# Optimization experiments

Measured on AMD Instinct MI355X. Metric: run time of the kernel, lower is better.

The kernel has to match this reference:

```python
import jax, jax.numpy as jnp
import numpy as np

TEMP = 0.07
MAX_SAMPLES = 2048
RADIUS = 10
HARD_FRAC = 0.75
FG_LABEL = 1
B, C, H, W = 8, 64, 256, 256
BLOCK = 32

MAX_FG = MAX_SAMPLES // 2                      # 1024
NEG_BUDGET = MAX_SAMPLES - MAX_FG              # 1024
HARD_BUDGET = int(round(HARD_FRAC * NEG_BUDGET))  # 768
RAND_BUDGET = NEG_BUDGET - HARD_BUDGET         # 256


def setup_inputs() -> dict:
    key = jax.random.key(0)
    feats = jax.random.normal(key, (B, C, H, W), dtype=jnp.float32)
    # 32x32-block checkerboard labels: guarantees abundant fg / ring / interior-bg pools
    ii, jj = jnp.meshgrid(jnp.arange(H), jnp.arange(W), indexing='ij')
    lbl = (((ii // BLOCK) + (jj // BLOCK)) % 2).astype(jnp.int32)
    labels = jnp.broadcast_to(lbl, (B, H, W))
    return {"feats": feats, "labels": labels}


def _forward(feats, labels):
    Bn, Cn, Hn, Wn = feats.shape
    n_pix = Hn * Wn
    f_flat = feats.reshape(Bn, Cn, n_pix).transpose(0, 2, 1)  # [B, P, C]
    l_flat = labels.reshape(Bn, n_pix)

    fg = labels == FG_LABEL                                   # [B, H, W]
    k = 2 * RADIUS + 1
    # max-pool dilation of fg mask (kernel k, stride 1, pad RADIUS == SAME)
    dil = jax.lax.reduce_window(fg.astype(jnp.float32), -jnp.inf, jax.lax.max,
                                (1, k, k), (1, 1, 1), 'SAME') > 0.0
    fg_flat = fg.reshape(Bn, n_pix)
    bg_flat = ~fg_flat                                        # all pixels valid (no ignore)
    ring_flat = dil.reshape(Bn, n_pix) & ~fg_flat & bg_flat
    bgonly_flat = bg_flat & ~ring_flat

    def per_image(f, y, fgm, ringm, bgm, key):
        k1, k2, k3 = jax.random.split(key, 3)
        def pick(mask, kk, n):
            # random subset of n true positions (== randperm[:n] in distribution)
            s = jnp.where(mask, jax.random.uniform(kk, mask.shape), -1.0)
            return jax.lax.top_k(s, n)[1]
        idx = jnp.concatenate([pick(fgm, k1, MAX_FG),
                               pick(ringm, k2, HARD_BUDGET),
                               pick(bgm, k3, RAND_BUDGET)])    # [K]
        fs = f[idx]                                            # [K, C]
        ys = y[idx]
        fs = fs / jnp.maximum(jnp.linalg.norm(fs, axis=1, keepdims=True), 1e-12)
        logits = fs @ fs.T / TEMP                              # [K, K]
        logits = logits - jax.lax.stop_gradient(logits.max(axis=1, keepdims=True))
        eye = jnp.eye(MAX_SAMPLES, dtype=bool)
        pos = (ys[:, None] == ys[None, :]) & ~eye
        exp_l = jnp.exp(logits) * (~eye)
        denom = jnp.maximum(exp_l.sum(axis=1), 1e-8)
        pos_sum = jnp.maximum(jnp.where(pos, exp_l, 0.0).sum(axis=1), 1e-8)
        valid = pos.any(axis=1) & (ys == FG_LABEL)
        loss_terms = -jnp.log(pos_sum / denom)
        n_valid = jnp.maximum(valid.sum(), 1)
        return jnp.where(valid, loss_terms, 0.0).sum() / n_valid

    keys = jax.random.split(jax.random.key(1), Bn)
    losses = jax.vmap(per_image)(f_flat, l_flat, fg_flat, ring_flat, bgonly_flat, keys)
    return losses.mean()


def reference(feats, labels):
    return _forward(feats, labels)
```

## Files before the change

### kernel.cpp

```cpp
#include <hip/hip_runtime.h>
#include <stdint.h>

#define NPIX   65536
#define NIMG   8
#define NCH    64
#define KSEL   2048
#define NFG    1024
#define NRING  768
#define NBG    256
#define INV_TEMP 14.285714285714286f

typedef __attribute__((ext_vector_type(8))) short bf16x8;
typedef __attribute__((ext_vector_type(4))) float f32x4;

__device__ __forceinline__ void tf2x32(uint32_t k0, uint32_t k1,
                                       uint32_t& x0, uint32_t& x1) {
  const uint32_t ks2 = k0 ^ k1 ^ 0x1BD11BDAu;
  x0 += k0; x1 += k1;
#define TF_RND(r) { x0 += x1; x1 = (x1 << (r)) | (x1 >> (32 - (r))); x1 ^= x0; }
  TF_RND(13) TF_RND(15) TF_RND(26) TF_RND(6)
  x0 += k1;  x1 += ks2 + 1u;
  TF_RND(17) TF_RND(29) TF_RND(16) TF_RND(24)
  x0 += ks2; x1 += k0 + 2u;
  TF_RND(13) TF_RND(15) TF_RND(26) TF_RND(6)
  x0 += k0;  x1 += k1 + 3u;
  TF_RND(17) TF_RND(29) TF_RND(16) TF_RND(24)
  x0 += k1;  x1 += ks2 + 4u;
  TF_RND(13) TF_RND(15) TF_RND(26) TF_RND(6)
  x0 += ks2; x1 += k0 + 5u;
#undef TF_RND
}

__device__ __forceinline__ ushort f2bf(float f) {
  uint32_t u = __float_as_uint(f);
  return (ushort)((u + 0x7FFFu + ((u >> 16) & 1u)) >> 16);
}

__global__ __launch_bounds__(256) void prep_hash(const int* __restrict__ labels,
                                                 float4* __restrict__ zreg,
                                                 uint32_t* __restrict__ mgrp,
                                                 uint32_t* __restrict__ hist32,
                                                 float* __restrict__ out) {
  __shared__ uint64_t fgs[112], hds[112], fgb[32], dlb[32];
  __shared__ uint32_t lh[768];
  __shared__ uint32_t skeys[6];
  const int tid = threadIdx.x;
  const int img = blockIdx.x >> 5;
  const int band = blockIdx.x & 31;

  if (blockIdx.x == 0) {
    if (tid < 16) zreg[tid] = make_float4(0.f, 0.f, 0.f, 0.f);
    if (tid == 0) out[0] = 0.0f;
  }

  if (tid < 3) {
    uint32_t kb0 = 0u, kb1 = (uint32_t)img;
    tf2x32(0u, 1u, kb0, kb1);
    uint32_t x0 = 0u, x1 = (uint32_t)tid;
    tf2x32(kb0, kb1, x0, x1);
    skeys[tid * 2 + 0] = x0;
    skeys[tid * 2 + 1] = x1;
  }
  for (int t = tid; t < 768; t += 256) lh[t] = 0;

  const int rbase = band * 8 - 10;
  for (int it = 0; it < 28; ++it) {
    int hr = rbase + it;
    bool bit = false;
    if (hr >= 0 && hr < 256) bit = (labels[(img << 16) + (hr << 8) + tid] == 1);
    uint64_t m = __ballot(bit);
    if ((tid & 63) == 0) fgs[it * 4 + (tid >> 6)] = m;
  }
  __syncthreads();

  for (int w = tid; w < 112; w += 256) {
    int wc = w & 3;
    uint64_t x = fgs[w];
    uint64_t L = wc > 0 ? fgs[w - 1] : 0ull;
    uint64_t R = wc < 3 ? fgs[w + 1] : 0ull;
    uint64_t acc = x;
    #pragma unroll
    for (int s = 1; s <= 10; ++s) {
      acc |= (x << s) | (L >> (64 - s));
      acc |= (x >> s) | (R << (64 - s));
    }
    hds[w] = acc;
  }
  __syncthreads();

  for (int w = tid; w < 32; w += 256) {
    int r = w >> 2, wc = w & 3;
    uint64_t acc = 0ull;
    #pragma unroll
    for (int dr = 0; dr <= 20; ++dr) acc |= hds[(r + dr) * 4 + wc];
    fgb[w] = fgs[(r + 10) * 4 + wc];
    dlb[w] = acc;
  }
  __syncthreads();

  const uint32_t K00 = skeys[0], K01 = skeys[1];
  const uint32_t K10 = skeys[2], K11 = skeys[3];
  const uint32_t K20 = skeys[4], K21 = skeys[5];
  const int pbase = blockIdx.x * 2048;

  #pragma unroll
  for (int k = 0; k < 8; ++k) {
    int off = k * 256 + tid;
    int pix = (pbase + off) & 65535;
    int lw = off >> 6, bp = off & 63;
    uint32_t fgbit = (uint32_t)((fgb[lw] >> bp) & 1ull);
    uint32_t dilbit = (uint32_t)((dlb[lw] >> bp) & 1ull);
    uint32_t grp = fgbit ? 0u : (dilbit ? 1u : 2u);
    uint32_t k0 = grp == 0 ? K00 : grp == 1 ? K10 : K20;
    uint32_t k1 = grp == 0 ? K01 : grp == 1 ? K11 : K21;
    uint32_t x0 = 0u, x1 = (uint32_t)pix;
    tf2x32(k0, k1, x0, x1);
    uint32_t m = (x0 ^ x1) >> 9;
    mgrp[pbase + off] = (m << 2) | grp;
    atomicAdd(&lh[grp * 256 + (m >> 15)], 1u);
  }
  __syncthreads();
  for (int t = tid; t < 768; t += 256) hist32[blockIdx.x * 768 + t] = lh[t];
}

__global__ __launch_bounds__(256) void topk_emit(const uint32_t* __restrict__ mgrp,
                                                 const uint32_t* __restrict__ hist32,
                                                 uint32_t* __restrict__ TG,
                                                 uint32_t* __restrict__ cnt,
                                                 uint32_t* __restrict__ candcnt,
                                                 unsigned long long* __restrict__ cand,
                                                 int* __restrict__ idx_out) {
  __shared__ uint32_t hh[768];
  __shared__ uint32_t sT[3], loc[3], lbd[3], basA[3], basB[3];
  const int tid = threadIdx.x;
  const int b = blockIdx.x >> 5;
  const int base = blockIdx.x * 2048;
  for (int t = tid; t < 768; t += 256) {
    uint32_t s = 0;
    const uint32_t* hp = hist32 + (size_t)b * 32 * 768 + t;
    #pragma unroll
    for (int band = 0; band < 32; ++band) s += hp[band * 768];
    hh[t] = s;
  }
  if (tid < 3) { loc[tid] = 0; lbd[tid] = 0; }
  __syncthreads();

  if (tid < 3) {
    uint32_t nsel = tid == 0 ? NFG : tid == 1 ? NRING : NBG;
    const uint32_t* h = hh + tid * 256;
    uint32_t cum = 0; int T = 255;
    for (; T > 0; --T) {
      uint32_t c = h[T];
      if (cum + c >= nsel) break;
      cum += c;
    }
    sT[tid] = (uint32_t)T;
    if ((blockIdx.x & 31) == 0) {
      TG[(b * 3 + tid) * 2] = (uint32_t)T;
      TG[(b * 3 + tid) * 2 + 1] = cum;
    }
  }
  __syncthreads();
  const uint32_t T0 = sT[0], T1 = sT[1], T2 = sT[2];

  #pragma unroll
  for (int k = 0; k < 8; ++k) {
    uint32_t v = mgrp[base + k * 256 + tid];
    uint32_t g = v & 3u, bin = v >> 17;
    uint32_t T = g == 0 ? T0 : g == 1 ? T1 : T2;
    if (bin > T) atomicAdd(&loc[g], 1u);
    else if (bin == T) atomicAdd(&lbd[g], 1u);
  }
  __syncthreads();
  if (tid < 3) {
    basA[tid] = atomicAdd(&cnt[b * 3 + tid], loc[tid]);
    basB[tid] = atomicAdd(&candcnt[b * 3 + tid], lbd[tid]);
    loc[tid] = 0; lbd[tid] = 0;
  }
  __syncthreads();

  #pragma unroll
  for (int k = 0; k < 8; ++k) {
    int p = base + k * 256 + tid;
    uint32_t v = mgrp[p];
    uint32_t g = v & 3u, bin = v >> 17;
    uint32_t T = g == 0 ? T0 : g == 1 ? T1 : T2;
    int pix = p & 65535;
    if (bin > T) {
      uint32_t o = atomicAdd(&loc[g], 1u);
      int seg = g == 0 ? 0 : g == 1 ? NFG : (NFG + NRING);
      idx_out[b * KSEL + seg + (int)(basA[g] + o)] = pix;
    } else if (bin == T) {
      uint32_t o = atomicAdd(&lbd[g], 1u);
      uint32_t c = basB[g] + o;
      uint32_t m = v >> 2;
      if (c < 1024u)
        cand[((size_t)b * 3 + g) * 1024 + c] =
            ((unsigned long long)m << 16) | (uint32_t)pix;
    }
  }
}

#define GA 16
__global__ __launch_bounds__(256) void gather_rank_t(
    const float* __restrict__ feats, const int* __restrict__ idx,
    const uint32_t* __restrict__ TG, const uint32_t* __restrict__ candcnt,
    const unsigned long long* __restrict__ cand, ushort* __restrict__ fs) {
  __shared__ float tile[GA * 65];
  __shared__ float ssb[16 * GA];
  __shared__ float sscale[GA];
  __shared__ int lidx[GA];
  __shared__ unsigned long long cb[1024];
  const int tid = threadIdx.x;
  const int img = blockIdx.x >> 7;
  const int win = (blockIdx.x & 127) * GA;
  int seg, segoff, nsel;
  if (win < NFG)               { seg = 0; segoff = 0;            nsel = NFG; }
  else if (win < NFG + NRING)  { seg = 1; segoff = NFG;          nsel = NRING; }
  else                         { seg = 2; segoff = NFG + NRING;  nsel = NBG; }
  const int task = img * 3 + seg;
  const uint32_t G = TG[task * 2 + 1];
  const int poslo = win - segoff;

  if (tid < GA) {
    if ((uint32_t)(poslo + tid) < G)
      lidx[tid] = idx[img * KSEL + win + tid];
  }
  const bool needRank = (uint32_t)(poslo + GA) > G;
  if (needRank) {
    const int c = (int)(candcnt[task] < 1024u ? candcnt[task] : 1024u);
    const int r = nsel - (int)G;
    for (int i = tid; i < c; i += 256) cb[i] = cand[task * 1024 + i];
    __syncthreads();
    for (int i = tid; i < c; i += 256) {
      unsigned long long me = cb[i];
      uint32_t mm = (uint32_t)(me >> 16), pi = (uint32_t)(me & 0xFFFFu);
      int rank = 0;
      for (int j = 0; j < c; ++j) {
        unsigned long long o = cb[j];
        uint32_t om = (uint32_t)(o >> 16), op = (uint32_t)(o & 0xFFFFu);
        if (om > mm || (om == mm && op < pi)) ++rank;
      }
      if (rank < r) {
        int slot = (int)G + rank - poslo;
        if (slot >= 0 && slot < GA) lidx[slot] = (int)pi;
      }
    }
  }
  __syncthreads();

  const int a = tid & 15, q = tid >> 4;
  const int pix = lidx[a];
  const float* fb = feats + ((size_t)img * NCH + q * 4) * NPIX + pix;
  float ss = 0.f;
  #pragma unroll
  for (int k = 0; k < 4; ++k) {
    float v = fb[(size_t)k * NPIX];
    tile[a * 65 + q * 4 + k] = v;
    ss += v * v;
  }
  ssb[q * GA + a] = ss;
  __syncthreads();
  if (q == 0) {
    float tot = 0.f;
    #pragma unroll
    for (int q2 = 0; q2 < 16; ++q2) tot += ssb[q2 * GA + a];
    sscale[a] = 1.0f / fmaxf(sqrtf(tot), 1e-12f);
  }
  __syncthreads();

  const int row = tid >> 4, c4 = tid & 15;
  const float sc = sscale[row];
  ushort4 v4;
  v4.x = f2bf(tile[row * 65 + c4 * 4 + 0] * sc);
  v4.y = f2bf(tile[row * 65 + c4 * 4 + 1] * sc);
  v4.z = f2bf(tile[row * 65 + c4 * 4 + 2] * sc);
  v4.w = f2bf(tile[row * 65 + c4 * 4 + 3] * sc);
  ((ushort4*)(fs + ((size_t)img * KSEL + win + row) * NCH))[c4] = v4;
}

__global__ __launch_bounds__(256) void loss_mfma(const ushort* __restrict__ fs,
                                                 float* __restrict__ out) {
  const int img = blockIdx.x & 7;
  const int a0 = (blockIdx.x >> 3) * 32;
  const ushort* X = fs + (size_t)img * KSEL * NCH;
  const int tid = threadIdx.x;
  const int lane = tid & 63, wave = tid >> 6;
  const int quad = lane >> 4, col = lane & 15;
  const int rt = wave >> 1, colh = wave & 1;

  __shared__ float redD[2][2][16];
  __shared__ float redP[2][16];

  const int arow = a0 + rt * 16 + col;
  const bf16x8* Ap = (const bf16x8*)(X + (size_t)arow * NCH + quad * 8);
  const bf16x8 a_lo = Ap[0];
  const bf16x8 a_hi = Ap[4];

  float pD[4] = {0.f, 0.f, 0.f, 0.f};
  float pP[4] = {0.f, 0.f, 0.f, 0.f};
  const int ct0 = colh * 64;
  const int mbase = a0 + rt * 16 + quad * 4;

  for (int ct = ct0; ct < ct0 + 64; ++ct) {
    const int j = ct * 16 + col;
    const bf16x8* Bp = (const bf16x8*)(X + (size_t)j * NCH + quad * 8);
    bf16x8 b_lo = Bp[0];
    bf16x8 b_hi = Bp[4];
    f32x4 d = {0.f, 0.f, 0.f, 0.f};
    d = __builtin_amdgcn_mfma_f32_16x16x32_bf16(a_lo, b_lo, d, 0, 0, 0);
    d = __builtin_amdgcn_mfma_f32_16x16x32_bf16(a_hi, b_hi, d, 0, 0, 0);
    #pragma unroll
    for (int r = 0; r < 4; ++r) {
      float e = __expf(d[r] * INV_TEMP);
      if (j == mbase + r) e = 0.f;
      pD[r] += e;
      if (colh == 0) pP[r] += e;
    }
  }

  #pragma unroll
  for (int o = 1; o < 16; o <<= 1) {
    #pragma unroll
    for (int r = 0; r < 4; ++r) {
      pD[r] += __shfl_xor(pD[r], o);
      pP[r] += __shfl_xor(pP[r], o);
    }
  }
  if (col == 0) {
    #pragma unroll
    for (int r = 0; r < 4; ++r) {
      redD[rt][colh][quad * 4 + r] = pD[r];
      if (colh == 0) redP[rt][quad * 4 + r] = pP[r];
    }
  }
  __syncthreads();

  float term = 0.f;
  if (tid < 32) {
    int lrt = tid >> 4, lr = tid & 15;
    float dsum = fmaxf(redD[lrt][0][lr] + redD[lrt][1][lr], 1e-8f);
    float psum = fmaxf(redP[lrt][lr], 1e-8f);
    term = __logf(dsum) - __logf(psum);
  }
  if (tid < 64) {
    #pragma unroll
    for (int o = 32; o > 0; o >>= 1) term += __shfl_xor(term, o);
    if (tid == 0) atomicAdd(out, term * (1.0f / (NFG * NIMG)));
  }
}

extern "C" void kernel_launch(void* const* d_in, const int* in_sizes, int n_in,
                              void* d_out, int out_size, void* d_ws, size_t ws_size,
                              hipStream_t stream) {
  const float* feats = (const float*)d_in[0];
  const int* labels  = (const int*)d_in[1];
  float* out = (float*)d_out;

  char* ws = (char*)d_ws;
  uint32_t* TG      = (uint32_t*)(ws);
  uint32_t* cnt     = (uint32_t*)(ws + 4096);
  uint32_t* candcnt = (uint32_t*)(ws + 4224);
  float4*   zreg    = (float4*)(ws + 4096);
  unsigned long long* cand = (unsigned long long*)(ws + 8192);
  int*      idx     = (int*)(ws + 262144);
  uint32_t* mgrp    = (uint32_t*)(ws + 2097152);
  uint32_t* hist32  = (uint32_t*)(ws + 4194304);
  ushort*   fs      = (ushort*)(ws + 8388608);

  hipLaunchKernelGGL(prep_hash, dim3(NIMG * 32), dim3(256), 0, stream,
                     labels, zreg, mgrp, hist32, out);
  hipLaunchKernelGGL(topk_emit, dim3(NIMG * 32), dim3(256), 0, stream,
                     mgrp, hist32, TG, cnt, candcnt, cand, idx);
  hipLaunchKernelGGL(gather_rank_t, dim3((NIMG * KSEL) / GA), dim3(256), 0, stream,
                     feats, idx, TG, candcnt, cand, fs);
  hipLaunchKernelGGL(loss_mfma, dim3(NIMG * (NFG / 32)), dim3(256), 0, stream,
                     fs, out);
}
```

Measured before the change: 239.9 us.

## Replace global atomic compaction with histogram prefix offsets and widen loss blocks

topk_emit now derives each band's output offsets from per-band histograms (a prefix over bands) and uses wave ballots plus popcount for ordered in-block compaction. This replaces the global atomic counters and the second pass over mgrp, and writes candcnt directly, so the zeroing of counters in prep_hash is dropped. loss_mfma moves to 1024-thread blocks with 8 column segments per row tile, giving each wave a quarter of the column loop to raise parallelism. The compaction adds two block barriers per iteration, and output order becomes deterministic.

```diff
diff --git a/kernel.cpp b/kernel.cpp
--- a/kernel.cpp
+++ b/kernel.cpp
@@ -37,7 +37,6 @@
 }
 
 __global__ __launch_bounds__(256) void prep_hash(const int* __restrict__ labels,
-                                                 float4* __restrict__ zreg,
                                                  uint32_t* __restrict__ mgrp,
                                                  uint32_t* __restrict__ hist32,
                                                  float* __restrict__ out) {
@@ -48,10 +47,7 @@
   const int img = blockIdx.x >> 5;
   const int band = blockIdx.x & 31;
 
-  if (blockIdx.x == 0) {
-    if (tid < 16) zreg[tid] = make_float4(0.f, 0.f, 0.f, 0.f);
-    if (tid == 0) out[0] = 0.0f;
-  }
+  if (blockIdx.x == 0 && tid == 0) out[0] = 0.0f;
 
   if (tid < 3) {
     uint32_t kb0 = 0u, kb1 = (uint32_t)img;
@@ -126,23 +122,31 @@
 __global__ __launch_bounds__(256) void topk_emit(const uint32_t* __restrict__ mgrp,
                                                  const uint32_t* __restrict__ hist32,
                                                  uint32_t* __restrict__ TG,
-                                                 uint32_t* __restrict__ cnt,
                                                  uint32_t* __restrict__ candcnt,
                                                  unsigned long long* __restrict__ cand,
                                                  int* __restrict__ idx_out) {
   __shared__ uint32_t hh[768];
-  __shared__ uint32_t sT[3], loc[3], lbd[3], basA[3], basB[3];
+  __shared__ uint32_t sT[3];
+  __shared__ uint32_t cA[3][32], cB[3][32];
+  __shared__ uint32_t preA[3], preB[3];
+  __shared__ uint32_t runA[3], runB[3];
+  __shared__ uint32_t wcA[3][4], wcB[3][4];
   const int tid = threadIdx.x;
   const int b = blockIdx.x >> 5;
+  const int band = blockIdx.x & 31;
   const int base = blockIdx.x * 2048;
+
+  uint32_t vv[8];
+  #pragma unroll
+  for (int k = 0; k < 8; ++k) vv[k] = mgrp[base + k * 256 + tid];
+
   for (int t = tid; t < 768; t += 256) {
     uint32_t s = 0;
-    const uint32_t* hp = hist32 + (size_t)b * 32 * 768 + t;
-    #pragma unroll
-    for (int band = 0; band < 32; ++band) s += hp[band * 768];
+    const uint32_t* hp = hist32 + (size_t)b * 24576 + t;
+    #pragma unroll
+    for (int bd = 0; bd < 32; ++bd) s += hp[bd * 768];
     hh[t] = s;
   }
-  if (tid < 3) { loc[tid] = 0; lbd[tid] = 0; }
   __syncthreads();
 
   if (tid < 3) {
@@ -155,49 +159,83 @@
       cum += c;
     }
     sT[tid] = (uint32_t)T;
-    if ((blockIdx.x & 31) == 0) {
+    runA[tid] = 0; runB[tid] = 0;
+    if (band == 0) {
       TG[(b * 3 + tid) * 2] = (uint32_t)T;
       TG[(b * 3 + tid) * 2 + 1] = cum;
+      candcnt[b * 3 + tid] = h[T];
     }
   }
   __syncthreads();
   const uint32_t T0 = sT[0], T1 = sT[1], T2 = sT[2];
 
-  #pragma unroll
+  if (tid < 96) {
+    int g = tid >> 5, bd = tid & 31;
+    uint32_t T = g == 0 ? T0 : g == 1 ? T1 : T2;
+    const uint32_t* hp = hist32 + (size_t)b * 24576 + bd * 768 + g * 256;
+    uint32_t sA = 0;
+    for (int t = (int)T + 1; t < 256; ++t) sA += hp[t];
+    cA[g][bd] = sA;
+    cB[g][bd] = hp[T];
+  }
+  __syncthreads();
+  if (tid < 3) {
+    uint32_t pa = 0, pb = 0;
+    for (int bd = 0; bd < band; ++bd) { pa += cA[tid][bd]; pb += cB[tid][bd]; }
+    preA[tid] = pa; preB[tid] = pb;
+  }
+  __syncthreads();
+
+  const int lane = tid & 63, w = tid >> 6;
+  #pragma unroll 1
   for (int k = 0; k < 8; ++k) {
-    uint32_t v = mgrp[base + k * 256 + tid];
-    uint32_t g = v & 3u, bin = v >> 17;
-    uint32_t T = g == 0 ? T0 : g == 1 ? T1 : T2;
-    if (bin > T) atomicAdd(&loc[g], 1u);
-    else if (bin == T) atomicAdd(&lbd[g], 1u);
-  }
-  __syncthreads();
-  if (tid < 3) {
-    basA[tid] = atomicAdd(&cnt[b * 3 + tid], loc[tid]);
-    basB[tid] = atomicAdd(&candcnt[b * 3 + tid], lbd[tid]);
-    loc[tid] = 0; lbd[tid] = 0;
-  }
-  __syncthreads();
-
-  #pragma unroll
-  for (int k = 0; k < 8; ++k) {
-    int p = base + k * 256 + tid;
-    uint32_t v = mgrp[p];
-    uint32_t g = v & 3u, bin = v >> 17;
-    uint32_t T = g == 0 ? T0 : g == 1 ? T1 : T2;
-    int pix = p & 65535;
-    if (bin > T) {
-      uint32_t o = atomicAdd(&loc[g], 1u);
-      int seg = g == 0 ? 0 : g == 1 ? NFG : (NFG + NRING);
-      idx_out[b * KSEL + seg + (int)(basA[g] + o)] = pix;
-    } else if (bin == T) {
-      uint32_t o = atomicAdd(&lbd[g], 1u);
-      uint32_t c = basB[g] + o;
-      uint32_t m = v >> 2;
-      if (c < 1024u)
-        cand[((size_t)b * 3 + g) * 1024 + c] =
-            ((unsigned long long)m << 16) | (uint32_t)pix;
-    }
+    const uint32_t v = vv[k];
+    const uint32_t g = v & 3u, bin = v >> 17;
+    const uint32_t T = g == 0 ? T0 : g == 1 ? T1 : T2;
+    const bool selA = bin > T;
+    const bool selB = bin == T;
+    const uint64_t mA0 = __ballot(selA && g == 0);
+    const uint64_t mA1 = __ballot(selA && g == 1);
+    const uint64_t mA2 = __ballot(selA && g == 2);
+    const uint64_t mB0 = __ballot(selB && g == 0);
+    const uint64_t mB1 = __ballot(selB && g == 1);
+    const uint64_t mB2 = __ballot(selB && g == 2);
+    if (lane == 0) {
+      wcA[0][w] = (uint32_t)__popcll(mA0);
+      wcA[1][w] = (uint32_t)__popcll(mA1);
+      wcA[2][w] = (uint32_t)__popcll(mA2);
+      wcB[0][w] = (uint32_t)__popcll(mB0);
+      wcB[1][w] = (uint32_t)__popcll(mB1);
+      wcB[2][w] = (uint32_t)__popcll(mB2);
+    }
+    __syncthreads();
+    if (selA || selB) {
+      const uint64_t mask = g == 0 ? (selA ? mA0 : mB0)
+                          : g == 1 ? (selA ? mA1 : mB1)
+                                   : (selA ? mA2 : mB2);
+      const uint32_t intra = (uint32_t)__popcll(mask & ((1ull << lane) - 1ull));
+      uint32_t wbase = 0;
+      for (int w2 = 0; w2 < w; ++w2) wbase += selA ? wcA[g][w2] : wcB[g][w2];
+      const int pix = (base + k * 256 + tid) & 65535;
+      if (selA) {
+        const uint32_t slot = preA[g] + runA[g] + wbase + intra;
+        const int seg = g == 0 ? 0 : g == 1 ? NFG : (NFG + NRING);
+        idx_out[b * KSEL + seg + (int)slot] = pix;
+      } else {
+        const uint32_t c = preB[g] + runB[g] + wbase + intra;
+        if (c < 1024u) {
+          const uint32_t m = v >> 2;
+          cand[((size_t)b * 3 + g) * 1024 + c] =
+              ((unsigned long long)m << 16) | (uint32_t)pix;
+        }
+      }
+    }
+    __syncthreads();
+    if (tid < 3) {
+      runA[tid] += wcA[tid][0] + wcA[tid][1] + wcA[tid][2] + wcA[tid][3];
+      runB[tid] += wcB[tid][0] + wcB[tid][1] + wcB[tid][2] + wcB[tid][3];
+    }
+    __syncthreads();
   }
 }
 
@@ -279,18 +317,18 @@
   ((ushort4*)(fs + ((size_t)img * KSEL + win + row) * NCH))[c4] = v4;
 }
 
-__global__ __launch_bounds__(256) void loss_mfma(const ushort* __restrict__ fs,
-                                                 float* __restrict__ out) {
+__global__ __launch_bounds__(1024) void loss_mfma(const ushort* __restrict__ fs,
+                                                  float* __restrict__ out) {
   const int img = blockIdx.x & 7;
   const int a0 = (blockIdx.x >> 3) * 32;
   const ushort* X = fs + (size_t)img * KSEL * NCH;
   const int tid = threadIdx.x;
   const int lane = tid & 63, wave = tid >> 6;
   const int quad = lane >> 4, col = lane & 15;
-  const int rt = wave >> 1, colh = wave & 1;
-
-  __shared__ float redD[2][2][16];
-  __shared__ float redP[2][16];
+  const int rt = wave >> 3, cseg = wave & 7;
+
+  __shared__ float redD[2][8][16];
+  __shared__ float redP[2][4][16];
 
   const int arow = a0 + rt * 16 + col;
   const bf16x8* Ap = (const bf16x8*)(X + (size_t)arow * NCH + quad * 8);
@@ -299,10 +337,10 @@
 
   float pD[4] = {0.f, 0.f, 0.f, 0.f};
   float pP[4] = {0.f, 0.f, 0.f, 0.f};
-  const int ct0 = colh * 64;
+  const int ct0 = cseg * 16;
   const int mbase = a0 + rt * 16 + quad * 4;
 
-  for (int ct = ct0; ct < ct0 + 64; ++ct) {
+  for (int ct = ct0; ct < ct0 + 16; ++ct) {
     const int j = ct * 16 + col;
     const bf16x8* Bp = (const bf16x8*)(X + (size_t)j * NCH + quad * 8);
     bf16x8 b_lo = Bp[0];
@@ -315,7 +353,7 @@
       float e = __expf(d[r] * INV_TEMP);
       if (j == mbase + r) e = 0.f;
       pD[r] += e;
-      if (colh == 0) pP[r] += e;
+      if (cseg < 4) pP[r] += e;
     }
   }
 
@@ -330,8 +368,8 @@
   if (col == 0) {
     #pragma unroll
     for (int r = 0; r < 4; ++r) {
-      redD[rt][colh][quad * 4 + r] = pD[r];
-      if (colh == 0) redP[rt][quad * 4 + r] = pP[r];
+      redD[rt][cseg][quad * 4 + r] = pD[r];
+      if (cseg < 4) redP[rt][cseg][quad * 4 + r] = pP[r];
     }
   }
   __syncthreads();
@@ -339,8 +377,13 @@
   float term = 0.f;
   if (tid < 32) {
     int lrt = tid >> 4, lr = tid & 15;
-    float dsum = fmaxf(redD[lrt][0][lr] + redD[lrt][1][lr], 1e-8f);
-    float psum = fmaxf(redP[lrt][lr], 1e-8f);
+    float dsum = 0.f, psum = 0.f;
+    #pragma unroll
+    for (int cs = 0; cs < 8; ++cs) dsum += redD[lrt][cs][lr];
+    #pragma unroll
+    for (int cs = 0; cs < 4; ++cs) psum += redP[lrt][cs][lr];
+    dsum = fmaxf(dsum, 1e-8f);
+    psum = fmaxf(psum, 1e-8f);
     term = __logf(dsum) - __logf(psum);
   }
   if (tid < 64) {
@@ -359,9 +402,7 @@
 
   char* ws = (char*)d_ws;
   uint32_t* TG      = (uint32_t*)(ws);
-  uint32_t* cnt     = (uint32_t*)(ws + 4096);
-  uint32_t* candcnt = (uint32_t*)(ws + 4224);
-  float4*   zreg    = (float4*)(ws + 4096);
+  uint32_t* candcnt = (uint32_t*)(ws + 4096);
   unsigned long long* cand = (unsigned long long*)(ws + 8192);
   int*      idx     = (int*)(ws + 262144);
   uint32_t* mgrp    = (uint32_t*)(ws + 2097152);
@@ -369,11 +410,11 @@
   ushort*   fs      = (ushort*)(ws + 8388608);
 
   hipLaunchKernelGGL(prep_hash, dim3(NIMG * 32), dim3(256), 0, stream,
-                     labels, zreg, mgrp, hist32, out);
+                     labels, mgrp, hist32, out);
   hipLaunchKernelGGL(topk_emit, dim3(NIMG * 32), dim3(256), 0, stream,
-                     mgrp, hist32, TG, cnt, candcnt, cand, idx);
+                     mgrp, hist32, TG, candcnt, cand, idx);
   hipLaunchKernelGGL(gather_rank_t, dim3((NIMG * KSEL) / GA), dim3(256), 0, stream,
                      feats, idx, TG, candcnt, cand, fs);
-  hipLaunchKernelGGL(loss_mfma, dim3(NIMG * (NFG / 32)), dim3(256), 0, stream,
+  hipLaunchKernelGGL(loss_mfma, dim3(NIMG * (NFG / 32)), dim3(1024), 0, stream,
                      fs, out);
 }
```

Measured after the change: 235.0 us, median of 2. 2.0% less time.
